# Kernel tuning notes

Hardware: AMD Instinct MI355X
Metric: run time of the kernel (lower is better)

Reference implementation:

```python
import jax, jax.numpy as jnp
import numpy as np

D_MODEL = 1024
D_STATE = 64
D_CONV = 4
EXPAND = 2
INNER = EXPAND * D_STATE          # 128
PROJ = D_STATE + 2 * INNER        # 320
B, L = 8, 4096
EPS = 1e-4


def setup_inputs() -> dict:
    key = jax.random.key(0)
    ks = jax.random.split(key, 6)
    x = jax.random.normal(ks[0], (B, L, D_MODEL), dtype=jnp.float32)
    # depthwise conv weight, torch layout (out=D, in/group=1, K)
    conv_w = jax.random.normal(ks[1], (D_MODEL, 1, D_CONV), dtype=jnp.float32) / np.sqrt(D_CONV)
    conv_b = jnp.zeros((D_MODEL,), dtype=jnp.float32)
    in_proj_w = jax.random.normal(ks[2], (PROJ, D_MODEL), dtype=jnp.float32) / np.sqrt(D_MODEL)
    in_proj_b = jnp.zeros((PROJ,), dtype=jnp.float32)
    A_log = jax.random.normal(ks[3], (D_STATE,), dtype=jnp.float32) * 0.1
    out_proj_w = jax.random.normal(ks[4], (D_MODEL, D_STATE), dtype=jnp.float32) / np.sqrt(D_STATE)
    out_proj_b = jnp.zeros((D_MODEL,), dtype=jnp.float32)
    return {"x": x, "conv_w": conv_w, "conv_b": conv_b,
            "in_proj_w": in_proj_w, "in_proj_b": in_proj_b,
            "A_log": A_log, "out_proj_w": out_proj_w, "out_proj_b": out_proj_b}


def _ssm_forward(x, conv_w, conv_b, in_proj_w, in_proj_b, A_log, out_proj_w, out_proj_b):
    bsz, L_in, _ = x.shape
    # depthwise conv1d, padding (D_CONV-1)//2 on both sides (torch semantics)
    pad = (D_CONV - 1) // 2
    xc = jnp.transpose(x, (0, 2, 1))  # (B, D, L)
    xc = jax.lax.conv_general_dilated(
        xc, conv_w, window_strides=(1,), padding=[(pad, pad)],
        dimension_numbers=("NCH", "OIH", "NCH"), feature_group_count=D_MODEL)
    xc = xc + conv_b[None, :, None]
    Lc = xc.shape[2]
    if Lc < L_in:  # K even -> conv output is L-1; pad zeros on the right
        xc = jnp.pad(xc, ((0, 0), (0, 0), (0, L_in - Lc)))
    elif Lc > L_in:
        xc = xc[:, :, :L_in]
    xc = jnp.transpose(xc, (0, 2, 1))  # (B, L, D)

    proj = xc @ in_proj_w.T + in_proj_b  # (B, L, PROJ)
    delta = proj[..., :D_STATE]                                  # (B, L, N)
    B_in = proj[..., D_STATE:D_STATE + INNER]
    C = proj[..., D_STATE + INNER:]
    n_groups = INNER // D_STATE
    B_in = B_in.reshape(bsz, L_in, D_STATE, n_groups).mean(axis=-1)  # (B, L, N)
    C = C.reshape(bsz, L_in, D_STATE, n_groups).mean(axis=-1)        # (B, L, N)

    # ZOH discretization
    A = -jnp.exp(A_log)[None, None, :]          # (1, 1, N)
    delta = jax.nn.softplus(delta)
    dA = delta * A
    A_bar = jnp.exp(dA)                         # (B, L, N)
    A_safe = jnp.where(jnp.abs(A) < EPS, EPS * jnp.sign(A) + EPS, A)
    scale = (A_bar - 1.0) / A_safe
    taylor = 1.0 + dA / 2.0 + dA * dA / 6.0
    scale = jnp.where(jnp.abs(A) < EPS, taylor, scale)
    B_bar = scale * B_in                        # (B, L, N)

    # linear recurrence h_t = A_bar_t * h_{t-1} + B_bar_t via associative scan
    def comb(e1, e2):
        a1, b1 = e1
        a2, b2 = e2
        return a1 * a2, a2 * b1 + b2
    _, h = jax.lax.associative_scan(comb, (A_bar, B_bar), axis=1)  # (B, L, N)

    y_state = C * h
    return y_state @ out_proj_w.T + out_proj_b  # (B, L, D)


def reference(x, conv_w, conv_b, in_proj_w, in_proj_b, A_log, out_proj_w, out_proj_b):
    return _ssm_forward(x, conv_w, conv_b, in_proj_w, in_proj_b, A_log, out_proj_w, out_proj_b)
```

## Files before the change

### kernel.cpp

```cpp
#include <hip/hip_runtime.h>
#include <cstdint>
#include <cstddef>

typedef __bf16 bf16;
typedef __attribute__((ext_vector_type(8))) __bf16 bf16x8;
typedef __attribute__((ext_vector_type(4))) float f32x4;

#define EPS_C 1e-4f
#define SWZ(r) (((r) ^ ((r) >> 2)) & 3)

#define BAR_LDS() do { asm volatile("s_waitcnt lgkmcnt(0)" ::: "memory"); \
                       __builtin_amdgcn_s_barrier(); } while (0)

__global__ __launch_bounds__(256) void k0_prep(const float* __restrict__ Wi,
    const float* __restrict__ Wo, bf16* __restrict__ Whg, bf16* __restrict__ Wlg,
    bf16* __restrict__ Wob, float* __restrict__ zpg)
{
    int idx = blockIdx.x * 256 + threadIdx.x;
    if (idx < 196608) {
        int nn = idx >> 10, k = idx & 1023;
        int wn = nn / 48, s = nn - wn * 48;
        if (s < 16) {
            int d = wn * 16 + s;
            float w = Wi[d * 1024 + k];
            bf16 h = (bf16)w;
            Whg[(k >> 5) * 6144 + nn * 32 + (k & 31)] = h;
            Wlg[(k >> 5) * 2048 + d * 32 + (k & 31)] = (bf16)(w - (float)h);
        } else if (s < 32) {
            int i = wn * 16 + (s - 16);
            float w = 0.5f * (Wi[(64 + 2 * i) * 1024 + k] + Wi[(65 + 2 * i) * 1024 + k]);
            Whg[(k >> 5) * 6144 + nn * 32 + (k & 31)] = (bf16)w;
        } else {
            int i = wn * 16 + (s - 32);
            float w = 0.5f * (Wi[(192 + 2 * i) * 1024 + k] + Wi[(193 + 2 * i) * 1024 + k]);
            Whg[(k >> 5) * 6144 + nn * 32 + (k & 31)] = (bf16)w;
        }
    } else if (idx < 262144) {
        int j = idx - 196608;
        Wob[j] = (bf16)Wo[j];
    } else {
        int j = idx - 262144;
        if (j < 1024) zpg[j] = 0.f;
    }
}

__global__ __launch_bounds__(256) void k1_convproj(
    const float* __restrict__ x, const float* __restrict__ conv_w,
    const float* __restrict__ conv_b, const float* __restrict__ in_proj_b,
    const float* __restrict__ A_log,
    const bf16* __restrict__ Whg, const bf16* __restrict__ Wlg,
    const float* __restrict__ zpg,
    float* __restrict__ Yp, float* __restrict__ Zp,
    float* __restrict__ Psum, float* __restrict__ Ssum)
{
    __shared__ char smem[52224];

    const int tid  = threadIdx.x;
    const int lane = tid & 63;
    const int wn   = tid >> 6;
    const int fr   = lane & 15, fs = lane >> 4;
    const int b    = blockIdx.x >> 6;
    const int tc   = blockIdx.x & 63;
    const int t0   = tc * 64;
    const int rot  = (blockIdx.x * 5) & 31;

    const int ct = tid >> 2, cs = tid & 3;
    const int gt = t0 + ct;
    const bool zrow = (gt == 4095);
    const int xwo = ct * 64 + (((cs ^ SWZ(ct)) & 3) << 4);

    int aoff[4];
#pragma unroll
    for (int mi = 0; mi < 4; ++mi) {
        int r = mi * 16 + fr;
        aoff[mi] = r * 64 + ((fs ^ SWZ(r)) << 4);
    }

    const float* rp[4];
#pragma unroll
    for (int dt = 0; dt < 4; ++dt) {
        int g = gt - 1 + dt;
        rp[dt] = (g >= 0 && g < 4096) ? (x + ((size_t)b * 4096 + g) * 1024 + cs * 8)
                                      : (zpg + cs * 8);
    }

    const size_t wfo  = (size_t)(wn * 48 + fr) * 32 + fs * 8;
    const size_t wfol = (size_t)(wn * 16 + fr) * 32 + fs * 8;

    {
        float* cwT = (float*)(smem + 16384);
        float* cbl = (float*)(smem + 32768);
        for (int p = tid; p < 1024; p += 256) {
            f32x4 w4 = *(const f32x4*)&conv_w[p * 4];
            cwT[p]        = w4.x;
            cwT[1024 + p] = w4.y;
            cwT[2048 + p] = w4.z;
            cwT[3072 + p] = w4.w;
        }
        ((f32x4*)cbl)[tid] = ((const f32x4*)conv_b)[tid];
    }

    f32x4  xr[4][2];
    bf16x8 wfh[3], wfl;
    f32x4  acc[4][3] = {};

    auto L = [&](int c) { return (c + rot) & 31; };

    auto fetch_x = [&](int lc) {
#pragma unroll
        for (int dt = 0; dt < 4; ++dt) {
            xr[dt][0] = *(const f32x4*)(rp[dt] + lc * 32);
            xr[dt][1] = *(const f32x4*)(rp[dt] + lc * 32 + 4);
        }
    };
    auto fetch_w = [&](int lc) {
        const bf16* ph = Whg + (size_t)lc * 6144 + wfo;
#pragma unroll
        for (int ni = 0; ni < 3; ++ni)
            wfh[ni] = *(const bf16x8*)(ph + ni * 512);
        wfl = *(const bf16x8*)(Wlg + (size_t)lc * 2048 + wfol);
    };
    auto conv = [&](int lc, int p) {
        char* xh = smem + p * 4096;
        char* xl = smem + 8192 + p * 4096;
        const float* cwT = (const float*)(smem + 16384);
        const float* cbl = (const float*)(smem + 32768);
        bf16x8 hi, lo;
#pragma unroll
        for (int s = 0; s < 2; ++s) {
            const int ch0 = lc * 32 + cs * 8 + s * 4;
            f32x4 w0 = *(const f32x4*)&cwT[ch0];
            f32x4 w1 = *(const f32x4*)&cwT[1024 + ch0];
            f32x4 w2 = *(const f32x4*)&cwT[2048 + ch0];
            f32x4 w3 = *(const f32x4*)&cwT[3072 + ch0];
            f32x4 bb = *(const f32x4*)&cbl[ch0];
#pragma unroll
            for (int j = 0; j < 4; ++j) {
                float v = bb[j];
                v = fmaf(w0[j], xr[0][s][j], v);
                v = fmaf(w1[j], xr[1][s][j], v);
                v = fmaf(w2[j], xr[2][s][j], v);
                v = fmaf(w3[j], xr[3][s][j], v);
                v = zrow ? 0.f : v;
                bf16 h = (bf16)v;
                hi[s * 4 + j] = h;
                lo[s * 4 + j] = (bf16)(v - (float)h);
            }
        }
        *(bf16x8*)(xh + xwo) = hi;
        *(bf16x8*)(xl + xwo) = lo;
    };

    fetch_x(L(0));
    fetch_w(L(0));
    __syncthreads();
    conv(L(0), 0);
    fetch_x(L(1));
    __syncthreads();

    auto body = [&](int c, int par) {
        const char* xh = smem + par * 4096;
        const char* xl = smem + 8192 + par * 4096;
        bf16x8 ah[4], al[4];
#pragma unroll
        for (int mi = 0; mi < 4; ++mi) {
            ah[mi] = *(const bf16x8*)(xh + aoff[mi]);
            al[mi] = *(const bf16x8*)(xl + aoff[mi]);
        }
        __builtin_amdgcn_s_setprio(1);
#pragma unroll
        for (int ni = 0; ni < 3; ++ni) {
            bf16x8 bh = wfh[ni];
#pragma unroll
            for (int mi = 0; mi < 4; ++mi)
                acc[mi][ni] = __builtin_amdgcn_mfma_f32_16x16x32_bf16(ah[mi], bh, acc[mi][ni], 0, 0, 0);
#pragma unroll
            for (int mi = 0; mi < 4; ++mi)
                acc[mi][ni] = __builtin_amdgcn_mfma_f32_16x16x32_bf16(al[mi], bh, acc[mi][ni], 0, 0, 0);
        }
#pragma unroll
        for (int mi = 0; mi < 4; ++mi)
            acc[mi][0] = __builtin_amdgcn_mfma_f32_16x16x32_bf16(ah[mi], wfl, acc[mi][0], 0, 0, 0);
        __builtin_amdgcn_s_setprio(0);
        if (c + 1 < 32) {
            fetch_w(L(c + 1));
            conv(L(c + 1), par ^ 1);
            if (c + 2 < 32) fetch_x(L(c + 2));
        }
        BAR_LDS();
    };

#pragma unroll 1
    for (int cc = 0; cc < 32; cc += 2) {
        body(cc,     0);
        body(cc + 1, 1);
    }

    float* res = (float*)smem;
#pragma unroll
    for (int mi = 0; mi < 4; ++mi)
#pragma unroll
        for (int ni = 0; ni < 3; ++ni) {
            int col = wn * 48 + ni * 16 + fr;
#pragma unroll
            for (int r = 0; r < 4; ++r)
                res[(mi * 16 + fs * 4 + r) * 196 + col] = acc[mi][ni][r];
        }
    __syncthreads();

    float* part = (float*)(smem + 50176);
    const int i  = lane;
    const int tg = tid >> 6;
    const float A  = -expf(A_log[i]);
    const float bd = in_proj_b[i];
    const float bB = 0.5f * (in_proj_b[64 + 2 * i] + in_proj_b[65 + 2 * i]);
    const float bC = 0.5f * (in_proj_b[192 + 2 * i] + in_proj_b[193 + 2 * i]);
    const bool tiny = fabsf(A) < EPS_C;
    const int dcol = (i >> 4) * 48 + (i & 15);
    float av[16], bv[16], cv[16];
#pragma unroll
    for (int r = 0; r < 16; ++r) {
        int t = tg * 16 + r;
        float d  = res[t * 196 + dcol] + bd;
        float Bm = res[t * 196 + dcol + 16] + bB;
        float Cm = res[t * 196 + dcol + 32] + bC;
        float delta = (d > 20.f) ? d : log1pf(expf(d));
        float dA = delta * A;
        float abar = expf(dA);
        float sc = tiny ? (1.f + dA * 0.5f + dA * dA * (1.f / 6.f)) : ((abar - 1.f) / A);
        av[r] = abar; bv[r] = sc * Bm; cv[r] = Cm;
    }
    float P = 1.f, S = 0.f;
#pragma unroll
    for (int r = 0; r < 16; ++r) { S = fmaf(av[r], S, bv[r]); P *= av[r]; }
    part[tg * 64 + i] = P;
    part[256 + tg * 64 + i] = S;
    __syncthreads();
    float h = 0.f, pp = 1.f;
#pragma unroll
    for (int g = 0; g < 3; ++g)
        if (g < tg) {
            float Pg = part[g * 64 + i], Sg = part[256 + g * 64 + i];
            h = fmaf(Pg, h, Sg);
            pp *= Pg;
        }
    size_t ob = ((size_t)b * 4096 + t0 + tg * 16) * 64 + i;
#pragma unroll
    for (int r = 0; r < 16; ++r) {
        h  = fmaf(av[r], h, bv[r]);
        pp *= av[r];
        Yp[ob + (size_t)r * 64] = cv[r] * h;
        Zp[ob + (size_t)r * 64] = cv[r] * pp;
    }
    if (tg == 3) {
        size_t o = ((size_t)b * 64 + tc) * 64 + i;
        Psum[o] = pp;
        Ssum[o] = h;
    }
}

__global__ __launch_bounds__(64) void k2_scan2(const float* __restrict__ Psum,
    const float* __restrict__ Ssum, float* __restrict__ Carry)
{
    int b = blockIdx.x, i = threadIdx.x;
    float Pv[64], Sv[64];
#pragma unroll
    for (int c = 0; c < 64; ++c) {
        size_t o = ((size_t)(b * 64) + c) * 64 + i;
        Pv[c] = Psum[o]; Sv[c] = Ssum[o];
    }
    float h = 0.f;
#pragma unroll
    for (int c = 0; c < 64; ++c) {
        size_t o = ((size_t)(b * 64) + c) * 64 + i;
        Carry[o] = h;
        h = fmaf(Pv[c], h, Sv[c]);
    }
}

__global__ __launch_bounds__(512) void k3_scan_out(
    const float* __restrict__ Yp, const float* __restrict__ Zp,
    const float* __restrict__ Carry, const bf16* __restrict__ Wob,
    const float* __restrict__ bo, float* __restrict__ out)
{
    __shared__ char sm3[8192];

    const int tid  = threadIdx.x;
    const int lane = tid & 63;
    const int wv   = tid >> 6;
    const int b    = blockIdx.x >> 6;
    const int ch   = blockIdx.x & 63;
    const int t0   = ch * 64;

    const int i = lane, tg = wv;
    float cr = Carry[((size_t)(b * 64) + ch) * 64 + i];
    size_t base = ((size_t)(b * 4096) + t0 + tg * 8) * 64 + i;
#pragma unroll
    for (int r = 0; r < 8; ++r) {
        float y = Yp[base + (size_t)r * 64] + Zp[base + (size_t)r * 64] * cr;
        int t = tg * 8 + r;
        int off = t * 128 + ((((i >> 3) ^ (t & 7)) & 7) << 4) + (i & 7) * 2;
        *(bf16*)(sm3 + off) = (bf16)y;
    }
    __syncthreads();

    const int fr = lane & 15, fs = lane >> 4;
    bf16x8 afr[4][2];
#pragma unroll
    for (int mi = 0; mi < 4; ++mi)
#pragma unroll
        for (int ks = 0; ks < 2; ++ks) {
            int row = mi * 16 + fr;
            int slot = ks * 4 + fs;
            int off = row * 128 + (((slot ^ (row & 7)) & 7) << 4);
            afr[mi][ks] = *(const bf16x8*)(sm3 + off);
        }
    const int n0 = wv * 128;
#pragma unroll
    for (int ni = 0; ni < 8; ++ni) {
        int col = n0 + ni * 16 + fr;
        bf16x8 b0 = *(const bf16x8*)(Wob + (size_t)col * 64 + fs * 8);
        bf16x8 b1 = *(const bf16x8*)(Wob + (size_t)col * 64 + 32 + fs * 8);
        float bias = bo[col];
#pragma unroll
        for (int mi = 0; mi < 4; ++mi) {
            f32x4 a = {};
            a = __builtin_amdgcn_mfma_f32_16x16x32_bf16(afr[mi][0], b0, a, 0, 0, 0);
            a = __builtin_amdgcn_mfma_f32_16x16x32_bf16(afr[mi][1], b1, a, 0, 0, 0);
#pragma unroll
            for (int r = 0; r < 4; ++r) {
                int t = mi * 16 + fs * 4 + r;
                out[((size_t)(b * 4096) + t0 + t) * 1024 + col] = a[r] + bias;
            }
        }
    }
}

extern "C" void kernel_launch(void* const* d_in, const int* in_sizes, int n_in,
                              void* d_out, int out_size, void* d_ws, size_t ws_size,
                              hipStream_t stream) {
    const float* x          = (const float*)d_in[0];
    const float* conv_w     = (const float*)d_in[1];
    const float* conv_b     = (const float*)d_in[2];
    const float* in_proj_w  = (const float*)d_in[3];
    const float* in_proj_b  = (const float*)d_in[4];
    const float* A_log      = (const float*)d_in[5];
    const float* out_proj_w = (const float*)d_in[6];
    const float* out_proj_b = (const float*)d_in[7];
    float* out = (float*)d_out;

    char* w = (char*)d_ws;
    bf16*  Whg  = (bf16*)w;
    bf16*  Wlg  = (bf16*)(w + 393216);
    bf16*  Wob  = (bf16*)(w + 524288);
    float* Yp   = (float*)(w + 655360);
    float* Zp   = (float*)(w + 9043968);
    float* Psum = (float*)(w + 17432576);
    float* Ssum = (float*)(w + 17563648);
    float* Carry= (float*)(w + 17694720);
    float* zpg  = (float*)(w + 17825792);

    hipLaunchKernelGGL(k0_prep,     dim3(1032), dim3(256), 0, stream,
                       in_proj_w, out_proj_w, Whg, Wlg, Wob, zpg);
    hipLaunchKernelGGL(k1_convproj, dim3(512),  dim3(256), 0, stream,
                       x, conv_w, conv_b, in_proj_b, A_log, Whg, Wlg, zpg,
                       Yp, Zp, Psum, Ssum);
    hipLaunchKernelGGL(k2_scan2,    dim3(8),    dim3(64),  0, stream, Psum, Ssum, Carry);
    hipLaunchKernelGGL(k3_scan_out, dim3(512),  dim3(512), 0, stream,
                       Yp, Zp, Carry, Wob, out_proj_b, out);
}
```

Baseline: 99.73 us.

## Compute two conv rows per thread to reuse overlapping x loads, pad LDS rows

Each thread now computes the depthwise conv for two adjacent time rows over 4 channels instead of one row over 8 channels. The two rows share taps, so a thread loads 5 x rows instead of 8 vectors. The LDS staging layout changes from XOR-swizzled 64-byte rows to 80-byte padded rows, which enlarges the buffers and shifts the conv-weight offsets. This cuts global load volume and register pressure in the conv stage. The cost is narrower 8-byte LDS stores and different bank-conflict behaviour on the MFMA operand reads.

```diff
diff --git a/kernel.cpp b/kernel.cpp
--- a/kernel.cpp
+++ b/kernel.cpp
@@ -3,6 +3,7 @@
 #include <cstddef>
 
 typedef __bf16 bf16;
+typedef __attribute__((ext_vector_type(4))) __bf16 bf16x4;
 typedef __attribute__((ext_vector_type(8))) __bf16 bf16x8;
 typedef __attribute__((ext_vector_type(4))) float f32x4;
 
@@ -64,32 +65,34 @@
     const int t0   = tc * 64;
     const int rot  = (blockIdx.x * 5) & 31;
 
-    const int ct = tid >> 2, cs = tid & 3;
-    const int gt = t0 + ct;
-    const bool zrow = (gt == 4095);
-    const int xwo = ct * 64 + (((cs ^ SWZ(ct)) & 3) << 4);
+    const int tp = tid >> 3, cq = tid & 7;
+    const int r0 = tp * 2, r1 = r0 + 1;
+    const int gt0 = t0 + r0;
+    const bool zrow1 = (gt0 + 1 == 4095);
+    const int woff0 = r0 * 80 + cq * 8;
+    const int woff1 = r1 * 80 + cq * 8;
 
     int aoff[4];
 #pragma unroll
     for (int mi = 0; mi < 4; ++mi) {
         int r = mi * 16 + fr;
-        aoff[mi] = r * 64 + ((fs ^ SWZ(r)) << 4);
-    }
-
-    const float* rp[4];
-#pragma unroll
-    for (int dt = 0; dt < 4; ++dt) {
-        int g = gt - 1 + dt;
-        rp[dt] = (g >= 0 && g < 4096) ? (x + ((size_t)b * 4096 + g) * 1024 + cs * 8)
-                                      : (zpg + cs * 8);
+        aoff[mi] = r * 80 + fs * 16;
+    }
+
+    const float* rp[5];
+#pragma unroll
+    for (int dt = 0; dt < 5; ++dt) {
+        int g = gt0 - 1 + dt;
+        rp[dt] = (g >= 0 && g < 4096) ? (x + ((size_t)b * 4096 + g) * 1024 + cq * 4)
+                                      : (zpg + cq * 4);
     }
 
     const size_t wfo  = (size_t)(wn * 48 + fr) * 32 + fs * 8;
     const size_t wfol = (size_t)(wn * 16 + fr) * 32 + fs * 8;
 
     {
-        float* cwT = (float*)(smem + 16384);
-        float* cbl = (float*)(smem + 32768);
+        float* cwT = (float*)(smem + 20480);
+        float* cbl = (float*)(smem + 36864);
         for (int p = tid; p < 1024; p += 256) {
             f32x4 w4 = *(const f32x4*)&conv_w[p * 4];
             cwT[p]        = w4.x;
@@ -100,7 +103,7 @@
         ((f32x4*)cbl)[tid] = ((const f32x4*)conv_b)[tid];
     }
 
-    f32x4  xr[4][2];
+    f32x4  xr[5];
     bf16x8 wfh[3], wfl;
     f32x4  acc[4][3] = {};
 
@@ -108,10 +111,8 @@
 
     auto fetch_x = [&](int lc) {
 #pragma unroll
-        for (int dt = 0; dt < 4; ++dt) {
-            xr[dt][0] = *(const f32x4*)(rp[dt] + lc * 32);
-            xr[dt][1] = *(const f32x4*)(rp[dt] + lc * 32 + 4);
-        }
+        for (int dt = 0; dt < 5; ++dt)
+            xr[dt] = *(const f32x4*)(rp[dt] + lc * 32);
     };
     auto fetch_w = [&](int lc) {
         const bf16* ph = Whg + (size_t)lc * 6144 + wfo;
@@ -121,34 +122,38 @@
         wfl = *(const bf16x8*)(Wlg + (size_t)lc * 2048 + wfol);
     };
     auto conv = [&](int lc, int p) {
-        char* xh = smem + p * 4096;
-        char* xl = smem + 8192 + p * 4096;
-        const float* cwT = (const float*)(smem + 16384);
-        const float* cbl = (const float*)(smem + 32768);
-        bf16x8 hi, lo;
-#pragma unroll
-        for (int s = 0; s < 2; ++s) {
-            const int ch0 = lc * 32 + cs * 8 + s * 4;
-            f32x4 w0 = *(const f32x4*)&cwT[ch0];
-            f32x4 w1 = *(const f32x4*)&cwT[1024 + ch0];
-            f32x4 w2 = *(const f32x4*)&cwT[2048 + ch0];
-            f32x4 w3 = *(const f32x4*)&cwT[3072 + ch0];
-            f32x4 bb = *(const f32x4*)&cbl[ch0];
-#pragma unroll
-            for (int j = 0; j < 4; ++j) {
-                float v = bb[j];
-                v = fmaf(w0[j], xr[0][s][j], v);
-                v = fmaf(w1[j], xr[1][s][j], v);
-                v = fmaf(w2[j], xr[2][s][j], v);
-                v = fmaf(w3[j], xr[3][s][j], v);
-                v = zrow ? 0.f : v;
-                bf16 h = (bf16)v;
-                hi[s * 4 + j] = h;
-                lo[s * 4 + j] = (bf16)(v - (float)h);
-            }
-        }
-        *(bf16x8*)(xh + xwo) = hi;
-        *(bf16x8*)(xl + xwo) = lo;
+        char* xh = smem + p * 5120;
+        char* xl = smem + 10240 + p * 5120;
+        const float* cwT = (const float*)(smem + 20480);
+        const float* cbl = (const float*)(smem + 36864);
+        const int ch0 = lc * 32 + cq * 4;
+        f32x4 w0 = *(const f32x4*)&cwT[ch0];
+        f32x4 w1 = *(const f32x4*)&cwT[1024 + ch0];
+        f32x4 w2 = *(const f32x4*)&cwT[2048 + ch0];
+        f32x4 w3 = *(const f32x4*)&cwT[3072 + ch0];
+        f32x4 bb = *(const f32x4*)&cbl[ch0];
+        bf16x4 hi0, lo0, hi1, lo1;
+#pragma unroll
+        for (int j = 0; j < 4; ++j) {
+            float v0 = bb[j];
+            v0 = fmaf(w0[j], xr[0][j], v0);
+            v0 = fmaf(w1[j], xr[1][j], v0);
+            v0 = fmaf(w2[j], xr[2][j], v0);
+            v0 = fmaf(w3[j], xr[3][j], v0);
+            float v1 = bb[j];
+            v1 = fmaf(w0[j], xr[1][j], v1);
+            v1 = fmaf(w1[j], xr[2][j], v1);
+            v1 = fmaf(w2[j], xr[3][j], v1);
+            v1 = fmaf(w3[j], xr[4][j], v1);
+            v1 = zrow1 ? 0.f : v1;
+            bf16 h0 = (bf16)v0, h1 = (bf16)v1;
+            hi0[j] = h0; lo0[j] = (bf16)(v0 - (float)h0);
+            hi1[j] = h1; lo1[j] = (bf16)(v1 - (float)h1);
+        }
+        *(bf16x4*)(xh + woff0) = hi0;
+        *(bf16x4*)(xh + woff1) = hi1;
+        *(bf16x4*)(xl + woff0) = lo0;
+        *(bf16x4*)(xl + woff1) = lo1;
     };
 
     fetch_x(L(0));
@@ -159,8 +164,8 @@
     __syncthreads();
 
     auto body = [&](int c, int par) {
-        const char* xh = smem + par * 4096;
-        const char* xl = smem + 8192 + par * 4096;
+        const char* xh = smem + par * 5120;
+        const char* xl = smem + 10240 + par * 5120;
         bf16x8 ah[4], al[4];
 #pragma unroll
         for (int mi = 0; mi < 4; ++mi) {
```

Result: faster. 95.78 us (-4.0%).
